# Performance work log

Measured on AMD Instinct MI355X. Metric: run time of the kernel, lower is better.

## Reference

```python
import jax, jax.numpy as jnp
import numpy as np

GRID_SIZE = 5
SPLINE_ORDER = 3
GRID_LO, GRID_HI = -1.0, 1.0


def _make_grid():
    # extended knot vector: grid_size + 2*spline_order intervals
    h = (GRID_HI - GRID_LO) / GRID_SIZE
    return jnp.arange(-SPLINE_ORDER, GRID_SIZE + SPLINE_ORDER + 1, dtype=jnp.float32) * h + GRID_LO


def _b_splines(x, grid):
    # x: [N, F] -> bases [N, F, GRID_SIZE + SPLINE_ORDER] via Cox-de Boor recursion
    xg = x[..., None]
    bases = ((xg >= grid[:-1]) & (xg < grid[1:])).astype(x.dtype)
    for k in range(1, SPLINE_ORDER + 1):
        left = (xg - grid[: -(k + 1)]) / (grid[k:-1] - grid[: -(k + 1)])
        right = (grid[k + 1:] - xg) / (grid[k + 1:] - grid[1:-k])
        bases = left * bases[..., :-1] + right * bases[..., 1:]
    return bases


def _kan_linear(x, base_w, spline_w, spline_scaler, grid):
    # x: [N, in], base_w: [out, in], spline_w: [out, in, K], spline_scaler: [out, in]
    base_out = jax.nn.relu(x) @ base_w.T
    n = x.shape[0]
    sw = (spline_w * spline_scaler[..., None]).reshape(base_w.shape[0], -1)  # [out, in*K]
    spline_out = _b_splines(x, grid).reshape(n, -1) @ sw.T
    return base_out + spline_out


def _kan_conv(x, base_w, spline_w, spline_scaler, grid, k=5):
    # x: [B, C, H, W] -> KANLinear over unfolded 5x5 patches (stride 1, VALID)
    B, C, H, W = x.shape
    patches = jax.lax.conv_general_dilated_patches(x, (k, k), (1, 1), 'VALID')  # [B, C*k*k, Ho, Wo]
    Ho, Wo = patches.shape[2], patches.shape[3]
    p = patches.transpose(0, 2, 3, 1).reshape(B * Ho * Wo, C * k * k)
    out = _kan_linear(p, base_w, spline_w, spline_scaler, grid)
    return out.reshape(B, Ho, Wo, -1).transpose(0, 3, 1, 2)


def _avgpool2(x):
    B, C, H, W = x.shape
    return x.reshape(B, C, H // 2, 2, W // 2, 2).mean(axis=(3, 5))


def setup_inputs() -> dict:
    key = jax.random.key(0)
    ks = jax.random.split(key, 13)
    s = 0.1
    return {
        'x': jax.random.normal(ks[0], (1024, 1, 28, 28), jnp.float32),
        'c1_base_w': jax.random.normal(ks[1], (6, 25), jnp.float32) * s,
        'c1_spline_w': jax.random.normal(ks[2], (6, 25, 8), jnp.float32) * s,
        'c1_spline_scaler': jax.random.normal(ks[3], (6, 25), jnp.float32) * s,
        'c2_base_w': jax.random.normal(ks[4], (16, 150), jnp.float32) * s,
        'c2_spline_w': jax.random.normal(ks[5], (16, 150, 8), jnp.float32) * s,
        'c2_spline_scaler': jax.random.normal(ks[6], (16, 150), jnp.float32) * s,
        'fc1_w': jax.random.normal(ks[7], (120, 256), jnp.float32) * s,
        'fc1_b': jax.random.normal(ks[8], (120,), jnp.float32) * s,
        'fc2_w': jax.random.normal(ks[9], (84, 120), jnp.float32) * s,
        'fc2_b': jax.random.normal(ks[10], (84,), jnp.float32) * s,
        'fc3_w': jax.random.normal(ks[11], (62, 84), jnp.float32) * s,
        'fc3_b': jax.random.normal(ks[12], (62,), jnp.float32) * s,
    }


def reference(x, c1_base_w, c1_spline_w, c1_spline_scaler,
              c2_base_w, c2_spline_w, c2_spline_scaler,
              fc1_w, fc1_b, fc2_w, fc2_b, fc3_w, fc3_b):
    grid = _make_grid()
    h = _kan_conv(x, c1_base_w, c1_spline_w, c1_spline_scaler, grid)   # [B,6,24,24]
    h = _avgpool2(h)                                                    # [B,6,12,12]
    h = _kan_conv(h, c2_base_w, c2_spline_w, c2_spline_scaler, grid)   # [B,16,8,8]
    h = _avgpool2(h)                                                    # [B,16,4,4]
    h = h.reshape(h.shape[0], -1)                                       # [B,256]
    h = jax.nn.relu(h @ fc1_w.T + fc1_b)
    h = jax.nn.relu(h @ fc2_w.T + fc2_b)
    return h @ fc3_w.T + fc3_b                                          # [B,62]
```

## Files before the change

kernel.cpp:

```cpp
#include <hip/hip_runtime.h>


typedef _Float16 f16;
typedef f16 f16x8 __attribute__((ext_vector_type(8)));
typedef float f32x4 __attribute__((ext_vector_type(4)));

#define ONE_SIXTH 0.16666666666666666f

__device__ __forceinline__ void spline9(float v, float* __restrict__ f) {
    float u  = 2.5f * v + 5.5f;
    bool valid = (u >= 0.0f) && (u < 11.0f);
    float fi = floorf(u);
    int   i  = (int)fi;
    float w  = u - fi;
    float omw = 1.0f - w;
    float w2 = w * w, w3 = w2 * w;
    float c0 = omw * omw * omw * ONE_SIXTH;
    float c1 = (3.0f * w3 - 6.0f * w2 + 4.0f) * ONE_SIXTH;
    float c2 = (-3.0f * w3 + 3.0f * w2 + 3.0f * w + 1.0f) * ONE_SIXTH;
    float c3 = w3 * ONE_SIXTH;
    int j0 = i - 3;
#pragma unroll
    for (int j = 0; j < 8; ++j) {
        int d = j - j0;
        float val = (d == 0) ? c0 : (d == 1) ? c1 : (d == 2) ? c2 : (d == 3) ? c3 : 0.0f;
        f[j] = valid ? val : 0.0f;
    }
    f[8] = fmaxf(v, 0.0f);
}

__device__ __forceinline__ void spline_chunks(float v, uint4& u0, uint4& u1) {
    float f[9];
    spline9(v, f);
    union { f16 h[8]; uint4 u; } a, b;
#pragma unroll
    for (int j = 0; j < 8; ++j) a.h[j] = (f16)f[j];
    b.u.x = 0u; b.u.y = 0u; b.u.z = 0u; b.u.w = 0u;
    b.h[0] = (f16)f[8];
    u0 = a.u; u1 = b.u;
}

__global__ __launch_bounds__(256) void k_prep(
    const float* __restrict__ c1_bw, const float* __restrict__ c1_sw,
    const float* __restrict__ c1_sc,
    const float* __restrict__ c2_bw, const float* __restrict__ c2_sw,
    const float* __restrict__ c2_sc,
    f16* __restrict__ W1g, f16* __restrict__ W2g)
{
    int t = blockIdx.x * 256 + threadIdx.x;
    if (t < 9216) {
        int tap = t >> 8, r = t & 255;
        int o = r >> 4, k = r & 15;
        float val = 0.0f;
        if (o < 6 && k < 9) {
            int ey = tap / 6, ex = tap - 6 * ey;
            float s = 0.0f;
            for (int a = 0; a < 2; ++a) {
                for (int b = 0; b < 2; ++b) {
                    int dy = ey - a, dx = ex - b;
                    if (dy >= 0 && dy < 5 && dx >= 0 && dx < 5) {
                        int idx = o * 25 + dy * 5 + dx;
                        s += (k == 8) ? c1_bw[idx] : c1_sw[idx * 8 + k] * c1_sc[idx];
                    }
                }
            }
            val = 0.25f * s;
        }
        W1g[t] = (f16)val;
    }
    if (t < 55296) {
        int c = t / 9216, r = t - c * 9216;
        int tap = r >> 8, rr = r & 255;
        int o = rr >> 4, k = rr & 15;
        float val = 0.0f;
        if (k < 9) {
            int ey = tap / 6, ex = tap - 6 * ey;
            float s = 0.0f;
            for (int a = 0; a < 2; ++a) {
                for (int b = 0; b < 2; ++b) {
                    int dy = ey - a, dx = ex - b;
                    if (dy >= 0 && dy < 5 && dx >= 0 && dx < 5) {
                        int idx = o * 150 + c * 25 + dy * 5 + dx;
                        s += (k == 8) ? c2_bw[idx] : c2_sw[idx * 8 + k] * c2_sc[idx];
                    }
                }
            }
            val = 0.25f * s;
        }
        W2g[t] = (f16)val;
    }
}

__global__ __launch_bounds__(192, 3) void k_conv12(
    const float* __restrict__ x, const f16* __restrict__ W1g,
    const f16* __restrict__ W2g, float* __restrict__ h2)
{
    __shared__ uint4  feat[1728];
    __shared__ float  h1l[864];
    __shared__ float4 rbuf[2][64];

    const int img = blockIdx.x;
    const int tid = threadIdx.x;
    const int lane = tid & 63, wv = tid >> 6;
    const int ln15 = lane & 15, g = lane >> 4;
    const int gh = g & 1, gt = g >> 1;

    {
        float xv[5];
#pragma unroll
        for (int p = 0; p < 5; ++p) {
            int e = tid + p * 192;
            xv[p] = x[img * 784 + (e < 784 ? e : 783)];
        }
#pragma unroll
        for (int p = 0; p < 5; ++p) {
            int e = tid + p * 192;
            if (e < 784) {
                uint4 u0, u1;
                spline_chunks(xv[p], u0, u1);
                int ch = e * 2;
                int q = (ch >> 3) & 7;
                feat[ch ^ q] = u0;
                feat[(ch + 1) ^ q] = u1;
            }
        }
    }
    __syncthreads();

    {
        int ebase[3];
#pragma unroll
        for (int t = 0; t < 3; ++t) {
            int p = (wv * 3 + t) * 16 + ln15;
            int py = p / 12, px = p - py * 12;
            ebase[t] = py * 56 + px * 2;
        }
        const f16* bbase = W1g + (gt * 16 + ln15) * 16 + gh * 8;
        f16x8 wreg[4];
#pragma unroll
        for (int i = 0; i < 4; ++i)
            wreg[i] = *(const f16x8*)(bbase + i * 512);

        f32x4 acc[3] = {{0,0,0,0},{0,0,0,0},{0,0,0,0}};

#pragma unroll
        for (int kc = 0; kc < 18; ++kc) {
            f16x8 bcur = wreg[kc & 3];
            wreg[kc & 3] = *(const f16x8*)(bbase + (kc + 4) * 512);
            int tap = kc * 2 + gt;
            int ey = (tap * 171) >> 10, ex = tap - ey * 6;
            int eoff = ey * 28 + ex;
#pragma unroll
            for (int t = 0; t < 3; ++t) {
                int ch = (ebase[t] + eoff) * 2 + gh;
                ch ^= (ch >> 3) & 7;
                f16x8 afrag = *(const f16x8*)(&feat[ch]);
                acc[t] = __builtin_amdgcn_mfma_f32_16x16x32_f16(afrag, bcur, acc[t], 0, 0, 0);
            }
        }
        if (ln15 < 6) {
#pragma unroll
            for (int t = 0; t < 3; ++t) {
                int p0 = (wv * 3 + t) * 16 + g * 4;
                *(float4*)&h1l[ln15 * 144 + p0] =
                    make_float4(acc[t][0], acc[t][1], acc[t][2], acc[t][3]);
            }
        }
    }
    __syncthreads();

    {
        float hv[5];
#pragma unroll
        for (int p = 0; p < 5; ++p) {
            int e = tid + p * 192;
            hv[p] = h1l[e < 864 ? e : 863];
        }
#pragma unroll
        for (int p = 0; p < 5; ++p) {
            int e = tid + p * 192;
            if (e < 864) {
                uint4 u0, u1;
                spline_chunks(hv[p], u0, u1);
                int ch = e * 2;
                int q = (ch >> 3) & 7;
                feat[ch ^ q] = u0;
                feat[(ch + 1) ^ q] = u1;
            }
        }
    }
    __syncthreads();

    {
        const int py = ln15 >> 2, px = ln15 & 3;
        const int epx = py * 24 + px * 2;
        const int kk0 = wv * 36;
        const f16* bbase = W2g + ((kk0 * 2 + gt) * 16 + ln15) * 16 + gh * 8;
        f16x8 wreg[4];
#pragma unroll
        for (int i = 0; i < 4; ++i)
            wreg[i] = *(const f16x8*)(bbase + i * 512);

        f32x4 accA = {0, 0, 0, 0}, accB = {0, 0, 0, 0};

#pragma unroll
        for (int i = 0; i < 36; ++i) {
            f16x8 bcur = wreg[i & 3];
            wreg[i & 3] = *(const f16x8*)(bbase + (i + 4) * 512);
            int c = 2 * wv + (i / 18);
            int tk = i - (i / 18) * 18;
            int tap = tk * 2 + gt;
            int ey = (tap * 171) >> 10, ex = tap - ey * 6;
            int elem = c * 144 + epx + ey * 12 + ex;
            int ch = elem * 2 + gh;
            ch ^= (ch >> 3) & 7;
            f16x8 afrag = *(const f16x8*)(&feat[ch]);
            if ((i & 1) == 0)
                accA = __builtin_amdgcn_mfma_f32_16x16x32_f16(afrag, bcur, accA, 0, 0, 0);
            else
                accB = __builtin_amdgcn_mfma_f32_16x16x32_f16(afrag, bcur, accB, 0, 0, 0);
        }
        f32x4 acc = accA + accB;

        if (wv) rbuf[wv - 1][lane] = make_float4(acc[0], acc[1], acc[2], acc[3]);
        __syncthreads();
        if (wv == 0) {
            float4 r0 = rbuf[0][lane], r1 = rbuf[1][lane];
            *(float4*)&h2[img * 256 + ln15 * 16 + g * 4] =
                make_float4(acc[0] + r0.x + r1.x, acc[1] + r0.y + r1.y,
                            acc[2] + r0.z + r1.z, acc[3] + r0.w + r1.w);
        }
    }
}

__global__ __launch_bounds__(256) void k_fc(
    const float* __restrict__ h2,
    const float* __restrict__ w1, const float* __restrict__ b1,
    const float* __restrict__ w2, const float* __restrict__ b2,
    const float* __restrict__ w3, const float* __restrict__ b3,
    float* __restrict__ out)
{
    __shared__ float xin[2][260];
    __shared__ float a1[2][120];
    __shared__ float a2[2][84];
    const int tid = threadIdx.x;
    const int r0 = blockIdx.x * 2;

    for (int i = tid; i < 512; i += 256)
        xin[i >> 8][i & 255] = h2[r0 * 256 + i];
    __syncthreads();

    if (tid < 240) {
        const int o = tid >> 1, r = tid & 1;
        const float* w = w1 + o * 256;
        float s = 0.0f;
#pragma unroll 8
        for (int k = 0; k < 64; ++k) {
            float4 wv = ((const float4*)w)[k];
            float4 xv = *(const float4*)(&xin[r][k * 4]);
            s += wv.x * xv.x + wv.y * xv.y + wv.z * xv.z + wv.w * xv.w;
        }
        a1[r][o] = fmaxf(s + b1[o], 0.0f);
    }
    __syncthreads();

    if (tid < 168) {
        const int o = tid >> 1, r = tid & 1;
        const float* w = w2 + o * 120;
        float s = 0.0f;
#pragma unroll
        for (int k = 0; k < 30; ++k) {
            float4 wv = ((const float4*)w)[k];
            float4 xv = *(const float4*)(&a1[r][k * 4]);
            s += wv.x * xv.x + wv.y * xv.y + wv.z * xv.z + wv.w * xv.w;
        }
        a2[r][o] = fmaxf(s + b2[o], 0.0f);
    }
    __syncthreads();

    if (tid < 124) {
        const int o = tid >> 1, r = tid & 1;
        const float* w = w3 + o * 84;
        float s = 0.0f;
#pragma unroll
        for (int k = 0; k < 21; ++k) {
            float4 wv = ((const float4*)w)[k];
            float4 xv = *(const float4*)(&a2[r][k * 4]);
            s += wv.x * xv.x + wv.y * xv.y + wv.z * xv.z + wv.w * xv.w;
        }
        out[(r0 + r) * 62 + o] = s + b3[o];
    }
}

extern "C" void kernel_launch(void* const* d_in, const int* in_sizes, int n_in,
                              void* d_out, int out_size, void* d_ws, size_t ws_size,
                              hipStream_t stream)
{
    (void)in_sizes; (void)n_in; (void)out_size; (void)ws_size;
    const float* x      = (const float*)d_in[0];
    const float* c1_bw  = (const float*)d_in[1];
    const float* c1_sw  = (const float*)d_in[2];
    const float* c1_sc  = (const float*)d_in[3];
    const float* c2_bw  = (const float*)d_in[4];
    const float* c2_sw  = (const float*)d_in[5];
    const float* c2_sc  = (const float*)d_in[6];
    const float* fc1_w  = (const float*)d_in[7];
    const float* fc1_b  = (const float*)d_in[8];
    const float* fc2_w  = (const float*)d_in[9];
    const float* fc2_b  = (const float*)d_in[10];
    const float* fc3_w  = (const float*)d_in[11];
    const float* fc3_b  = (const float*)d_in[12];
    float* out = (float*)d_out;

    char* wsb = (char*)d_ws;
    f16*   W1g = (f16*)(wsb);
    f16*   W2g = (f16*)(wsb + 18432);
    float* h2  = (float*)(wsb + 131072);

    hipLaunchKernelGGL(k_prep, dim3(256), dim3(256), 0, stream,
                       c1_bw, c1_sw, c1_sc, c2_bw, c2_sw, c2_sc, W1g, W2g);
    hipLaunchKernelGGL(k_conv12, dim3(1024), dim3(192), 0, stream,
                       x, W1g, W2g, h2);
    hipLaunchKernelGGL(k_fc, dim3(512), dim3(256), 0, stream,
                       h2, fc1_w, fc1_b, fc2_w, fc2_b, fc3_w, fc3_b, out);
}
```

Measured before the change: 39.60 us.

## Give each wave private spline-feature regions to drop block barriers; batch 4 rows in FC

The conv kernel now has each wavefront build the spline features for only the input rows and channels it consumes, writing them into its own slice of shared memory. That removes two block-wide barriers between building the features and running the MFMA loops. The cost is that conv1 halo rows are recomputed per wave and the shared feature buffer grows. Separately, the FC kernel handles four batch rows per block instead of two, halving the block count and reusing each weight load across more rows.

```diff
diff --git a/kernel.cpp b/kernel.cpp
--- a/kernel.cpp
+++ b/kernel.cpp
@@ -95,7 +95,7 @@
     const float* __restrict__ x, const f16* __restrict__ W1g,
     const f16* __restrict__ W2g, float* __restrict__ h2)
 {
-    __shared__ uint4  feat[1728];
+    __shared__ uint4  feat[2016];
     __shared__ float  h1l[864];
     __shared__ float4 rbuf[2][64];
 
@@ -106,26 +106,28 @@
     const int gh = g & 1, gt = g >> 1;
 
     {
-        float xv[5];
-#pragma unroll
-        for (int p = 0; p < 5; ++p) {
-            int e = tid + p * 192;
-            xv[p] = x[img * 784 + (e < 784 ? e : 783)];
-        }
-#pragma unroll
-        for (int p = 0; p < 5; ++p) {
-            int e = tid + p * 192;
-            if (e < 784) {
+        const int r0 = 8 * wv;
+        float xv[6];
+#pragma unroll
+        for (int p = 0; p < 6; ++p) {
+            int e = lane + p * 64;
+            int ee = e < 336 ? e : 335;
+            int row = ee / 28, col = ee - row * 28;
+            xv[p] = x[img * 784 + (r0 + row) * 28 + col];
+        }
+#pragma unroll
+        for (int p = 0; p < 6; ++p) {
+            int e = lane + p * 64;
+            if (e < 336) {
                 uint4 u0, u1;
                 spline_chunks(xv[p], u0, u1);
-                int ch = e * 2;
+                int ch = wv * 672 + e * 2;
                 int q = (ch >> 3) & 7;
                 feat[ch ^ q] = u0;
                 feat[(ch + 1) ^ q] = u1;
             }
         }
     }
-    __syncthreads();
 
     {
         int ebase[3];
@@ -133,7 +135,8 @@
         for (int t = 0; t < 3; ++t) {
             int p = (wv * 3 + t) * 16 + ln15;
             int py = p / 12, px = p - py * 12;
-            ebase[t] = py * 56 + px * 2;
+            int row_local = 2 * py - 8 * wv;
+            ebase[t] = row_local * 28 + 2 * px;
         }
         const f16* bbase = W1g + (gt * 16 + ln15) * 16 + gh * 8;
         f16x8 wreg[4];
@@ -152,7 +155,7 @@
             int eoff = ey * 28 + ex;
 #pragma unroll
             for (int t = 0; t < 3; ++t) {
-                int ch = (ebase[t] + eoff) * 2 + gh;
+                int ch = wv * 672 + (ebase[t] + eoff) * 2 + gh;
                 ch ^= (ch >> 3) & 7;
                 f16x8 afrag = *(const f16x8*)(&feat[ch]);
                 acc[t] = __builtin_amdgcn_mfma_f32_16x16x32_f16(afrag, bcur, acc[t], 0, 0, 0);
@@ -173,23 +176,23 @@
         float hv[5];
 #pragma unroll
         for (int p = 0; p < 5; ++p) {
-            int e = tid + p * 192;
-            hv[p] = h1l[e < 864 ? e : 863];
+            int e = lane + p * 64;
+            int ee = e < 288 ? e : 287;
+            hv[p] = h1l[wv * 288 + ee];
         }
 #pragma unroll
         for (int p = 0; p < 5; ++p) {
-            int e = tid + p * 192;
-            if (e < 864) {
+            int e = lane + p * 64;
+            if (e < 288) {
                 uint4 u0, u1;
                 spline_chunks(hv[p], u0, u1);
-                int ch = e * 2;
+                int ch = wv * 576 + e * 2;
                 int q = (ch >> 3) & 7;
                 feat[ch ^ q] = u0;
                 feat[(ch + 1) ^ q] = u1;
             }
         }
     }
-    __syncthreads();
 
     {
         const int py = ln15 >> 2, px = ln15 & 3;
@@ -207,12 +210,12 @@
         for (int i = 0; i < 36; ++i) {
             f16x8 bcur = wreg[i & 3];
             wreg[i & 3] = *(const f16x8*)(bbase + (i + 4) * 512);
-            int c = 2 * wv + (i / 18);
-            int tk = i - (i / 18) * 18;
+            int cl = i / 18;
+            int tk = i - cl * 18;
             int tap = tk * 2 + gt;
             int ey = (tap * 171) >> 10, ex = tap - ey * 6;
-            int elem = c * 144 + epx + ey * 12 + ex;
-            int ch = elem * 2 + gh;
+            int elem = cl * 144 + epx + ey * 12 + ex;
+            int ch = wv * 576 + elem * 2 + gh;
             ch ^= (ch >> 3) & 7;
             f16x8 afrag = *(const f16x8*)(&feat[ch]);
             if ((i & 1) == 0)
@@ -240,18 +243,18 @@
     const float* __restrict__ w3, const float* __restrict__ b3,
     float* __restrict__ out)
 {
-    __shared__ float xin[2][260];
-    __shared__ float a1[2][120];
-    __shared__ float a2[2][84];
+    __shared__ float xin[4][260];
+    __shared__ float a1[4][120];
+    __shared__ float a2[4][84];
     const int tid = threadIdx.x;
-    const int r0 = blockIdx.x * 2;
-
-    for (int i = tid; i < 512; i += 256)
+    const int r0 = blockIdx.x * 4;
+
+    for (int i = tid; i < 1024; i += 256)
         xin[i >> 8][i & 255] = h2[r0 * 256 + i];
     __syncthreads();
 
-    if (tid < 240) {
-        const int o = tid >> 1, r = tid & 1;
+    for (int idx = tid; idx < 480; idx += 256) {
+        const int o = idx >> 2, r = idx & 3;
         const float* w = w1 + o * 256;
         float s = 0.0f;
 #pragma unroll 8
@@ -264,8 +267,8 @@
     }
     __syncthreads();
 
-    if (tid < 168) {
-        const int o = tid >> 1, r = tid & 1;
+    for (int idx = tid; idx < 336; idx += 256) {
+        const int o = idx >> 2, r = idx & 3;
         const float* w = w2 + o * 120;
         float s = 0.0f;
 #pragma unroll
@@ -278,8 +281,8 @@
     }
     __syncthreads();
 
-    if (tid < 124) {
-        const int o = tid >> 1, r = tid & 1;
+    for (int idx = tid; idx < 248; idx += 256) {
+        const int o = idx >> 2, r = idx & 3;
         const float* w = w3 + o * 84;
         float s = 0.0f;
 #pragma unroll
@@ -315,12 +318,12 @@
     char* wsb = (char*)d_ws;
     f16*   W1g = (f16*)(wsb);
     f16*   W2g = (f16*)(wsb + 18432);
-    float* h2  = (float*)(wsb + 131072);
+    float* h2  = (float*)(wsb + 139264);
 
     hipLaunchKernelGGL(k_prep, dim3(256), dim3(256), 0, stream,
                        c1_bw, c1_sw, c1_sc, c2_bw, c2_sw, c2_sc, W1g, W2g);
     hipLaunchKernelGGL(k_conv12, dim3(1024), dim3(192), 0, stream,
                        x, W1g, W2g, h2);
-    hipLaunchKernelGGL(k_fc, dim3(512), dim3(256), 0, stream,
+    hipLaunchKernelGGL(k_fc, dim3(256), dim3(256), 0, stream,
                        h2, fc1_w, fc1_b, fc2_w, fc2_b, fc3_w, fc3_b, out);
 }
```

New measurement: 39.13 us, median of 2. No clear change (-1.2%).
